# Kernel tuning notes

Hardware: AMD Instinct MI355X
Metric: run time of the kernel (lower is better)

## Reference

```python
import jax, jax.numpy as jnp
import numpy as np

FS = 48000          # sample_rate
C = 343.0           # sound speed
MAX_ORDER = 10
T = 24000           # RIR buffer length
W = 81              # fractional-delay sinc filter length
HALF = W // 2
BETA = 0.9          # wall reflection coefficient
OFFSET = 40.0       # global delay offset (matches shoebox_origin = 40 + fs*d/c)
NEG_SLOPE = 0.01    # torch LeakyReLU default


def _mlp(x, W1, b1, W2, b2, W3, b3):
    h = jax.nn.leaky_relu(x @ W1.T + b1, NEG_SLOPE)
    h = jax.nn.leaky_relu(h @ W2.T + b2, NEG_SLOPE)
    return jax.nn.sigmoid(h @ W3.T + b3)  # [B, 9]


def _image_source_rir(room, mic, src):
    """Batched shoebox image-source RIR synthesis with windowed-sinc scatter.

    room, mic, src: [B, 3]. Returns rir: [B, T].
    """
    B = room.shape[0]
    k = jnp.arange(-MAX_ORDER, MAX_ORDER + 1)          # [K], K = 21
    even = (k % 2 == 0)

    def axis_images(a):
        L = room[:, a:a + 1]                           # [B, 1]
        s = src[:, a:a + 1]                            # [B, 1]
        # even k: k*L + s ; odd k: (k+1)*L - s  (standard 1-D mirror images)
        return jnp.where(even[None, :], k[None, :] * L + s,
                         (k[None, :] + 1) * L - s)     # [B, K]

    ix, iy, iz = axis_images(0), axis_images(1), axis_images(2)
    dx = ix[:, :, None, None] - mic[:, 0, None, None, None]
    dy = iy[:, None, :, None] - mic[:, 1, None, None, None]
    dz = iz[:, None, None, :] - mic[:, 2, None, None, None]
    d = jnp.sqrt(dx * dx + dy * dy + dz * dz)          # [B, K, K, K]

    ka = jnp.abs(k)
    order = (ka[:, None, None] + ka[None, :, None] + ka[None, None, :])  # [K,K,K]

    d = d.reshape(B, -1)                               # [B, K^3]
    order_f = order.reshape(-1).astype(d.dtype)        # [K^3]
    valid_order = order.reshape(-1) <= MAX_ORDER

    amp = jnp.where(valid_order[None, :],
                    (BETA ** order_f)[None, :] / (4.0 * jnp.pi * jnp.maximum(d, 1e-3)),
                    0.0)                               # [B, K^3]

    delay = OFFSET + FS * d / C                        # fractional sample delay
    t0 = jnp.floor(delay)
    frac = delay - t0                                  # grad flows through delay
    t0 = t0.astype(jnp.int32)

    j = jnp.arange(W)
    hann = 0.5 * (1.0 - jnp.cos(2.0 * jnp.pi * j / (W - 1)))
    # windowed fractional-delay sinc taps: [B, K^3, W]
    taps = jnp.sinc((j - HALF)[None, None, :].astype(d.dtype) - frac[..., None]) * hann
    vals = amp[..., None] * taps                       # [B, K^3, W]

    idx = t0[..., None] + (j - HALF)                   # [B, K^3, W]
    in_range = (idx >= 0) & (idx < T)
    vals = jnp.where(in_range, vals, 0.0)
    idx = jnp.clip(idx, 0, T - 1)

    b = jnp.arange(B)[:, None, None]
    return jnp.zeros((B, T), vals.dtype).at[b, idx].add(vals)


def setup_inputs() -> dict:
    key = jax.random.key(0)
    ks = jax.random.split(key, 7)
    B = 128
    inp = {
        "input": jax.random.normal(ks[0], (B, 22), dtype=jnp.float32),
        "W1": jax.random.normal(ks[1], (30, 22), dtype=jnp.float32) * 0.2,
        "b1": jax.random.normal(ks[2], (30,), dtype=jnp.float32) * 0.05,
        "W2": jax.random.normal(ks[3], (20, 30), dtype=jnp.float32) * 0.2,
        "b2": jax.random.normal(ks[4], (20,), dtype=jnp.float32) * 0.05,
        "W3": jax.random.normal(ks[5], (9, 20), dtype=jnp.float32) * 0.2,
        "b3": jax.random.normal(ks[6], (9,), dtype=jnp.float32) * 0.05,
    }
    return inp


def reference(input, W1, b1, W2, b2, W3, b3):
    z = _mlp(input, W1, b1, W2, b2, W3, b3)            # [B, 9] in (0,1)
    room = z[:, 0:3] * 20.0                            # room dims in (0, 20) m
    mic = z[:, 3:6] * room                             # mic inside room
    src = z[:, 6:9] * room                             # source inside room
    rir = _image_source_rir(room, mic, src)            # [B, 24000]
    dist = jnp.linalg.norm(mic - src, axis=1)          # [B]
    origin = 40.0 + FS * dist / C                      # [B]
    return rir, origin
```

## Files before the change

### kernel.cpp

```cpp
#include <hip/hip_runtime.h>
#include <math.h>

#define T_LEN      24000
#define W_LEN      81
#define HALF_W     40
#define NK         21
#define MAXORD     10
#define NIMG_TOTAL 1561
#define NROUNDS    25
#define NB         376
#define GSAMP      128
#define NGRP       188
#define FS_F       48000.0f
#define C_F        343.0f
#define FS_OVER_C  (48000.0f / 343.0f)
#define PI_F       3.14159265358979323846f
#define HSTEP      (2.0f * PI_F / 80.0f)
#define INV_4PI_F  0.07957747154594767f
#define LOG2_BETA  (-0.15200309344504997f)
#define NEG_SLOPE  0.01f

#define HDR_I      384
#define ROW_BYTES  (HDR_I * 4 + 1600 * 16)

struct Table { unsigned int e[NROUNDS * 64]; };
constexpr Table make_table() {
    Table t{};
    int n = 0;
    for (int kx = 0; kx < NK; ++kx)
        for (int ky = 0; ky < NK; ++ky)
            for (int kz = 0; kz < NK; ++kz) {
                int ax = kx >= MAXORD ? kx - MAXORD : MAXORD - kx;
                int ay = ky >= MAXORD ? ky - MAXORD : MAXORD - ky;
                int az = kz >= MAXORD ? kz - MAXORD : MAXORD - kz;
                int order = ax + ay + az;
                if (order <= MAXORD)
                    t.e[n++] = (unsigned)((order << 15) | (kx << 10) | (ky << 5) | kz);
            }
    for (int i = n; i < NROUNDS * 64; ++i) t.e[i] = t.e[n - 1];
    return t;
}
__constant__ Table g_tbl = make_table();

__global__ __launch_bounds__(64)
void rir_prep_kernel(const float* __restrict__ g_in,
                     const float* __restrict__ W1, const float* __restrict__ b1,
                     const float* __restrict__ W2, const float* __restrict__ b2,
                     const float* __restrict__ W3, const float* __restrict__ b3,
                     unsigned char* __restrict__ ws, float* __restrict__ out_origin)
{
    __shared__ float dsq[3 * NK];
    __shared__ float h1[30], h2[20], zb[9], sm_in[22], rms[9];
    __shared__ int counts[NB], offs[NB + 1], cursor[NB];

    const int lane = threadIdx.x;
    const int b    = blockIdx.x;

    for (int i = lane; i < NB; i += 64) { counts[i] = 0; cursor[i] = 0; }

    if (lane < 22) sm_in[lane] = g_in[b * 22 + lane];
    if (lane < 30) {
        float a = b1[lane];
        const float* wp = W1 + lane * 22;
        #pragma unroll
        for (int i = 0; i < 22; ++i) a += sm_in[i] * wp[i];
        h1[lane] = (a >= 0.0f) ? a : NEG_SLOPE * a;
    }
    if (lane < 20) {
        float a = b2[lane];
        const float* wp = W2 + lane * 30;
        #pragma unroll
        for (int i = 0; i < 30; ++i) a += h1[i] * wp[i];
        h2[lane] = (a >= 0.0f) ? a : NEG_SLOPE * a;
    }
    if (lane < 9) {
        float a = b3[lane];
        const float* wp = W3 + lane * 20;
        #pragma unroll
        for (int i = 0; i < 20; ++i) a += h2[i] * wp[i];
        zb[lane] = 1.0f / (1.0f + __expf(-a));
    }
    if (lane < 3) {
        float room = zb[lane] * 20.0f;
        rms[lane]     = room;
        rms[3 + lane] = zb[3 + lane] * room;
        rms[6 + lane] = zb[6 + lane] * room;
    }
    if (lane == 0) {
        float dx = rms[3] - rms[6], dy = rms[4] - rms[7], dz = rms[5] - rms[8];
        out_origin[b] = 40.0f + FS_F * sqrtf(dx * dx + dy * dy + dz * dz) / C_F;
    }
    if (lane < 3 * NK) {
        int a  = lane / NK;
        int kk = (lane - a * NK) - MAXORD;
        float L = rms[a], src = rms[6 + a];
        float img = ((kk & 1) == 0) ? (float)kk * L + src : (float)(kk + 1) * L - src;
        float diff = img - rms[3 + a];
        dsq[lane] = diff * diff;
    }

    for (int r = 0; r < NROUNDS; ++r) {
        int gi = r * 64 + lane;
        unsigned e = g_tbl.e[gi];
        int kzi = e & 31, kyi = (e >> 5) & 31, kxi = (e >> 10) & 31;
        float d   = sqrtf(dsq[kxi] + dsq[NK + kyi] + dsq[2 * NK + kzi]);
        float dly = 40.0f + d * FS_OVER_C;
        int   t0  = (int)floorf(dly);
        bool live = (gi < NIMG_TOTAL) && (t0 - HALF_W < T_LEN);
        if (live) atomicAdd(&counts[t0 >> 6], 1);
    }
    if (lane == 0) {
        int acc = 0;
        for (int s = 0; s < NB; ++s) { offs[s] = acc; acc += counts[s]; }
        offs[NB] = acc;
    }

    unsigned char* rowp = ws + (size_t)b * ROW_BYTES;
    int*    hdr  = (int*)rowp;
    float4* prow = (float4*)(rowp + HDR_I * 4);

    for (int r = 0; r < NROUNDS; ++r) {
        int gi = r * 64 + lane;
        unsigned e = g_tbl.e[gi];
        int kzi = e & 31, kyi = (e >> 5) & 31, kxi = (e >> 10) & 31, order = (int)(e >> 15);
        float d   = sqrtf(dsq[kxi] + dsq[NK + kyi] + dsq[2 * NK + kzi]);
        float dly = 40.0f + d * FS_OVER_C;
        float t0f = floorf(dly);
        int   t0  = (int)t0f;
        bool live = (gi < NIMG_TOTAL) && (t0 - HALF_W < T_LEN);
        if (live) {
            float frac = dly - t0f;
            float amp  = exp2f((float)order * LOG2_BETA) * INV_4PI_F
                         * __builtin_amdgcn_rcpf(fmaxf(d, 0.001f));
            float sp   = __sinf(PI_F * frac);
            int rank = offs[t0 >> 6] + atomicAdd(&cursor[t0 >> 6], 1);
            prow[rank] = make_float4(amp, frac, sp, t0f);
        }
    }

    for (int i = lane; i <= NB; i += 64) hdr[i] = offs[i];
}

__global__ __launch_bounds__(256)
void rir_gather4_kernel(const unsigned char* __restrict__ ws,
                        float* __restrict__ out_rir)
{
    __shared__ float buf[GSAMP];

    const int tid  = threadIdx.x;
    const int lane = tid & 63;
    const int w    = tid >> 6;
    const int grp  = blockIdx.x;
    const int b    = blockIdx.y;
    const int g0   = grp * GSAMP;

    const unsigned char* rowp = ws + (size_t)b * ROW_BYTES;
    const int*    hdr  = (const int*)rowp;
    const float4* prow = (const float4*)(rowp + HDR_I * 4);

    const int blo   = max(g0 - HALF_W, 0) >> 6;
    const int bhi   = min(g0 + GSAMP - 1 + HALF_W, T_LEN + HALF_W - 1) >> 6;
    const int start = hdr[blo];
    const int end   = hdr[bhi + 1];

    if (tid < GSAMP) buf[tid] = 0.0f;
    __syncthreads();

    float acc0 = 0.0f, acc1 = 0.0f;
    const float gf0 = (float)(g0 + lane);

    for (int i = start + w; i < end; i += 4) {
        float4 p = prow[i];
        float n0 = gf0 - p.w;
        float n1 = n0 + 64.0f;

        if (fabsf(n0) <= 40.0f) {
            float x  = n0 - p.y;
            int   ni = (int)n0;
            float sg = (ni & 1) ? p.z : -p.z;
            float sv = (x == 0.0f) ? 1.0f : sg * __builtin_amdgcn_rcpf(PI_F * x);
            float hj = 0.5f - 0.5f * __cosf((n0 + 40.0f) * HSTEP);
            acc0 += p.x * sv * hj;
        }
        if (fabsf(n1) <= 40.0f) {
            float x  = n1 - p.y;
            int   ni = (int)n1;
            float sg = (ni & 1) ? p.z : -p.z;
            float sv = (x == 0.0f) ? 1.0f : sg * __builtin_amdgcn_rcpf(PI_F * x);
            float hj = 0.5f - 0.5f * __cosf((n1 + 40.0f) * HSTEP);
            acc1 += p.x * sv * hj;
        }
    }

    if (acc0 != 0.0f) atomicAdd(&buf[lane], acc0);
    if (acc1 != 0.0f) atomicAdd(&buf[lane + 64], acc1);
    __syncthreads();

    const int g = g0 + tid;
    if (tid < GSAMP && g < T_LEN)
        out_rir[(size_t)b * T_LEN + g] = buf[tid];
}

#define FTS 448
#define FNSLICE 54
__global__ __launch_bounds__(64)
void rir_wave_kernel(const float* __restrict__ g_in,
                     const float* __restrict__ W1, const float* __restrict__ b1,
                     const float* __restrict__ W2, const float* __restrict__ b2,
                     const float* __restrict__ W3, const float* __restrict__ b3,
                     float* __restrict__ out_rir, float* __restrict__ out_origin)
{
    __shared__ __align__(16) float rirw[FTS];
    __shared__ float dsq[3 * NK];
    __shared__ float h1[30], h2[20], zb[9], sm_in[22], rms[9];

    const int lane = threadIdx.x;
    const int s    = blockIdx.x;
    const int b    = blockIdx.y;
    const int lo   = s * FTS;
    const int nout = min(FTS, T_LEN - lo);

    float4* rir4 = (float4*)rirw;
    rir4[lane] = make_float4(0.f, 0.f, 0.f, 0.f);
    if (lane < FTS / 4 - 64) rir4[64 + lane] = make_float4(0.f, 0.f, 0.f, 0.f);

    const float c1p = PI_F * (float)(lane - HALF_W);
    const float hw1 = 0.5f - 0.5f * __cosf((float)lane * HSTEP);
    const float hw2 = 0.5f - 0.5f * __cosf((float)(lane + 64) * HSTEP);
    const float sg  = (lane & 1) ? 1.0f : -1.0f;

    if (lane < 22) sm_in[lane] = g_in[b * 22 + lane];
    if (lane < 30) {
        float a = b1[lane];
        const float* wp = W1 + lane * 22;
        #pragma unroll
        for (int i = 0; i < 22; ++i) a += sm_in[i] * wp[i];
        h1[lane] = (a >= 0.0f) ? a : NEG_SLOPE * a;
    }
    if (lane < 20) {
        float a = b2[lane];
        const float* wp = W2 + lane * 30;
        #pragma unroll
        for (int i = 0; i < 30; ++i) a += h1[i] * wp[i];
        h2[lane] = (a >= 0.0f) ? a : NEG_SLOPE * a;
    }
    if (lane < 9) {
        float a = b3[lane];
        const float* wp = W3 + lane * 20;
        #pragma unroll
        for (int i = 0; i < 20; ++i) a += h2[i] * wp[i];
        zb[lane] = 1.0f / (1.0f + __expf(-a));
    }
    if (lane < 3) {
        float room = zb[lane] * 20.0f;
        rms[lane]     = room;
        rms[3 + lane] = zb[3 + lane] * room;
        rms[6 + lane] = zb[6 + lane] * room;
    }
    if (lane == 0 && s == 0) {
        float dx = rms[3] - rms[6], dy = rms[4] - rms[7], dz = rms[5] - rms[8];
        out_origin[b] = 40.0f + FS_F * sqrtf(dx * dx + dy * dy + dz * dz) / C_F;
    }
    if (lane < 3 * NK) {
        int a  = lane / NK;
        int kk = (lane - a * NK) - MAXORD;
        float L = rms[a], src = rms[6 + a];
        float img = ((kk & 1) == 0) ? (float)kk * L + src : (float)(kk + 1) * L - src;
        float diff = img - rms[3 + a];
        dsq[lane] = diff * diff;
    }

    const float lof = (float)(lo - HALF_W);
    const float hif = (float)(lo + nout - 1 + HALF_W);

    for (int r = 0; r < NROUNDS; ++r) {
        unsigned e = g_tbl.e[r * 64 + lane];
        bool live  = (r * 64 + lane) < NIMG_TOTAL;
        int kzi = e & 31, kyi = (e >> 5) & 31, kxi = (e >> 10) & 31, order = (int)(e >> 15);
        float d    = sqrtf(dsq[kxi] + dsq[NK + kyi] + dsq[2 * NK + kzi]);
        float dlyv = 40.0f + d * FS_OVER_C;
        float t0f  = floorf(dlyv);
        float ampv = exp2f((float)order * LOG2_BETA) * INV_4PI_F
                     * __builtin_amdgcn_rcpf(fmaxf(d, 0.001f));
        bool hit = live && (t0f >= lof) && (t0f <= hif);

        unsigned long long mask = __ballot(hit);
        while (mask) {
            int l0 = __builtin_ctzll(mask); mask &= mask - 1;
            float a0 = __shfl(ampv, l0), d0 = __shfl(dlyv, l0);
            float t0b  = floorf(d0);
            float frac = d0 - t0b;
            float sp   = __sinf(PI_F * frac);
            float pv   = sg * sp;
            int   idx  = (int)t0b - HALF_W + lane - lo;
            float x1p  = c1p - PI_F * frac;
            float sv1  = (x1p == 0.0f) ? 1.0f : pv * __builtin_amdgcn_rcpf(x1p);
            if ((unsigned)idx < (unsigned)nout)
                atomicAdd(&rirw[idx], a0 * sv1 * hw1);
            if (lane < 17) {
                int idx2 = idx + 64;
                float sv2 = pv * __builtin_amdgcn_rcpf(x1p + 64.0f * PI_F);
                if ((unsigned)idx2 < (unsigned)nout)
                    atomicAdd(&rirw[idx2], a0 * sv2 * hw2);
            }
        }
    }

    const int n4 = nout / 4;
    float4* out4 = (float4*)(out_rir + (size_t)b * T_LEN + lo);
    out4[lane] = rir4[lane];
    if (lane + 64 < n4) out4[lane + 64] = rir4[lane + 64];
}

extern "C" void kernel_launch(void* const* d_in, const int* in_sizes, int n_in,
                              void* d_out, int out_size, void* d_ws, size_t ws_size,
                              hipStream_t stream) {
    const float* g_in = (const float*)d_in[0];
    const float* W1   = (const float*)d_in[1];
    const float* b1   = (const float*)d_in[2];
    const float* W2   = (const float*)d_in[3];
    const float* b2   = (const float*)d_in[4];
    const float* W3   = (const float*)d_in[5];
    const float* b3   = (const float*)d_in[6];

    const int B = in_sizes[0] / 22;

    float* out_rir    = (float*)d_out;
    float* out_origin = out_rir + (size_t)B * T_LEN;

    const size_t need_ws = (size_t)B * ROW_BYTES;

    if (ws_size >= need_ws) {
        unsigned char* ws = (unsigned char*)d_ws;
        rir_prep_kernel<<<B, 64, 0, stream>>>(
            g_in, W1, b1, W2, b2, W3, b3, ws, out_origin);
        dim3 grid2(NGRP, B);
        rir_gather4_kernel<<<grid2, 256, 0, stream>>>(ws, out_rir);
    } else {
        dim3 grid(FNSLICE, B);
        rir_wave_kernel<<<grid, 64, 0, stream>>>(
            g_in, W1, b1, W2, b2, W3, b3, out_rir, out_origin);
    }
}
```

Baseline: 73.50 us.

## Widen prep kernel to four waves, parallel scan, and precompute Hann table in gather

The prep kernel now runs with 256 threads, so its rounds are split across four waves, and the serial single-lane prefix sum over the bins is replaced by a wave-level shuffle scan. The record stored per image now holds amp*sin(pi*frac) and amp, which removes a multiply per tap in the gather. The gather kernel builds an 81-entry Hann window in shared memory and looks it up instead of evaluating cosine per tap, and its loop is unrolled by two. Adding __syncthreads barriers fixes ordering that the single-wave version got implicitly, at the cost of barrier overhead and extra shared-memory reads.

```diff
diff --git a/kernel.cpp b/kernel.cpp
--- a/kernel.cpp
+++ b/kernel.cpp
@@ -42,7 +42,7 @@
 }
 __constant__ Table g_tbl = make_table();
 
-__global__ __launch_bounds__(64)
+__global__ __launch_bounds__(256)
 void rir_prep_kernel(const float* __restrict__ g_in,
                      const float* __restrict__ W1, const float* __restrict__ b1,
                      const float* __restrict__ W2, const float* __restrict__ b2,
@@ -53,53 +53,58 @@
     __shared__ float h1[30], h2[20], zb[9], sm_in[22], rms[9];
     __shared__ int counts[NB], offs[NB + 1], cursor[NB];
 
-    const int lane = threadIdx.x;
+    const int tid  = threadIdx.x;
+    const int lane = tid & 63;
+    const int w    = tid >> 6;
     const int b    = blockIdx.x;
 
-    for (int i = lane; i < NB; i += 64) { counts[i] = 0; cursor[i] = 0; }
-
-    if (lane < 22) sm_in[lane] = g_in[b * 22 + lane];
-    if (lane < 30) {
-        float a = b1[lane];
-        const float* wp = W1 + lane * 22;
-        #pragma unroll
-        for (int i = 0; i < 22; ++i) a += sm_in[i] * wp[i];
-        h1[lane] = (a >= 0.0f) ? a : NEG_SLOPE * a;
-    }
-    if (lane < 20) {
-        float a = b2[lane];
-        const float* wp = W2 + lane * 30;
-        #pragma unroll
-        for (int i = 0; i < 30; ++i) a += h1[i] * wp[i];
-        h2[lane] = (a >= 0.0f) ? a : NEG_SLOPE * a;
-    }
-    if (lane < 9) {
-        float a = b3[lane];
-        const float* wp = W3 + lane * 20;
-        #pragma unroll
-        for (int i = 0; i < 20; ++i) a += h2[i] * wp[i];
-        zb[lane] = 1.0f / (1.0f + __expf(-a));
-    }
-    if (lane < 3) {
-        float room = zb[lane] * 20.0f;
-        rms[lane]     = room;
-        rms[3 + lane] = zb[3 + lane] * room;
-        rms[6 + lane] = zb[6 + lane] * room;
-    }
-    if (lane == 0) {
-        float dx = rms[3] - rms[6], dy = rms[4] - rms[7], dz = rms[5] - rms[8];
-        out_origin[b] = 40.0f + FS_F * sqrtf(dx * dx + dy * dy + dz * dz) / C_F;
-    }
-    if (lane < 3 * NK) {
-        int a  = lane / NK;
-        int kk = (lane - a * NK) - MAXORD;
-        float L = rms[a], src = rms[6 + a];
-        float img = ((kk & 1) == 0) ? (float)kk * L + src : (float)(kk + 1) * L - src;
-        float diff = img - rms[3 + a];
-        dsq[lane] = diff * diff;
-    }
-
-    for (int r = 0; r < NROUNDS; ++r) {
+    for (int i = tid; i < NB; i += 256) { counts[i] = 0; cursor[i] = 0; }
+
+    if (w == 0) {
+        if (lane < 22) sm_in[lane] = g_in[b * 22 + lane];
+        if (lane < 30) {
+            float a = b1[lane];
+            const float* wp = W1 + lane * 22;
+            #pragma unroll
+            for (int i = 0; i < 22; ++i) a += sm_in[i] * wp[i];
+            h1[lane] = (a >= 0.0f) ? a : NEG_SLOPE * a;
+        }
+        if (lane < 20) {
+            float a = b2[lane];
+            const float* wp = W2 + lane * 30;
+            #pragma unroll
+            for (int i = 0; i < 30; ++i) a += h1[i] * wp[i];
+            h2[lane] = (a >= 0.0f) ? a : NEG_SLOPE * a;
+        }
+        if (lane < 9) {
+            float a = b3[lane];
+            const float* wp = W3 + lane * 20;
+            #pragma unroll
+            for (int i = 0; i < 20; ++i) a += h2[i] * wp[i];
+            zb[lane] = 1.0f / (1.0f + __expf(-a));
+        }
+        if (lane < 3) {
+            float room = zb[lane] * 20.0f;
+            rms[lane]     = room;
+            rms[3 + lane] = zb[3 + lane] * room;
+            rms[6 + lane] = zb[6 + lane] * room;
+        }
+        if (lane == 0) {
+            float dx = rms[3] - rms[6], dy = rms[4] - rms[7], dz = rms[5] - rms[8];
+            out_origin[b] = 40.0f + FS_F * sqrtf(dx * dx + dy * dy + dz * dz) / C_F;
+        }
+        if (lane < 3 * NK) {
+            int a  = lane / NK;
+            int kk = (lane - a * NK) - MAXORD;
+            float L = rms[a], src = rms[6 + a];
+            float img = ((kk & 1) == 0) ? (float)kk * L + src : (float)(kk + 1) * L - src;
+            float diff = img - rms[3 + a];
+            dsq[lane] = diff * diff;
+        }
+    }
+    __syncthreads();
+
+    for (int r = w; r < NROUNDS; r += 4) {
         int gi = r * 64 + lane;
         unsigned e = g_tbl.e[gi];
         int kzi = e & 31, kyi = (e >> 5) & 31, kxi = (e >> 10) & 31;
@@ -109,17 +114,39 @@
         bool live = (gi < NIMG_TOTAL) && (t0 - HALF_W < T_LEN);
         if (live) atomicAdd(&counts[t0 >> 6], 1);
     }
-    if (lane == 0) {
-        int acc = 0;
-        for (int s = 0; s < NB; ++s) { offs[s] = acc; acc += counts[s]; }
-        offs[NB] = acc;
-    }
+    __syncthreads();
+
+    if (w == 0) {
+        const int base = lane * 6;
+        int c[6], s0 = 0;
+        #pragma unroll
+        for (int j = 0; j < 6; ++j) {
+            int idx = base + j;
+            c[j] = (idx < NB) ? counts[idx] : 0;
+            s0 += c[j];
+        }
+        int incl = s0;
+        #pragma unroll
+        for (int off = 1; off < 64; off <<= 1) {
+            int t = __shfl_up(incl, off);
+            if (lane >= off) incl += t;
+        }
+        int acc = incl - s0;
+        #pragma unroll
+        for (int j = 0; j < 6; ++j) {
+            int idx = base + j;
+            if (idx < NB) offs[idx] = acc;
+            acc += c[j];
+        }
+        if (lane == 63) offs[NB] = acc;
+    }
+    __syncthreads();
 
     unsigned char* rowp = ws + (size_t)b * ROW_BYTES;
     int*    hdr  = (int*)rowp;
     float4* prow = (float4*)(rowp + HDR_I * 4);
 
-    for (int r = 0; r < NROUNDS; ++r) {
+    for (int r = w; r < NROUNDS; r += 4) {
         int gi = r * 64 + lane;
         unsigned e = g_tbl.e[gi];
         int kzi = e & 31, kyi = (e >> 5) & 31, kxi = (e >> 10) & 31, order = (int)(e >> 15);
@@ -134,11 +161,12 @@
                          * __builtin_amdgcn_rcpf(fmaxf(d, 0.001f));
             float sp   = __sinf(PI_F * frac);
             int rank = offs[t0 >> 6] + atomicAdd(&cursor[t0 >> 6], 1);
-            prow[rank] = make_float4(amp, frac, sp, t0f);
-        }
-    }
-
-    for (int i = lane; i <= NB; i += 64) hdr[i] = offs[i];
+            prow[rank] = make_float4(amp * sp, frac, amp, t0f);
+        }
+    }
+    __syncthreads();
+
+    for (int i = tid; i <= NB; i += 256) hdr[i] = offs[i];
 }
 
 __global__ __launch_bounds__(256)
@@ -146,6 +174,7 @@
                         float* __restrict__ out_rir)
 {
     __shared__ float buf[GSAMP];
+    __shared__ float hann[W_LEN + 7];
 
     const int tid  = threadIdx.x;
     const int lane = tid & 63;
@@ -164,11 +193,14 @@
     const int end   = hdr[bhi + 1];
 
     if (tid < GSAMP) buf[tid] = 0.0f;
+    if (tid >= 128 && tid < 128 + W_LEN)
+        hann[tid - 128] = 0.5f - 0.5f * __cosf((float)(tid - 128) * HSTEP);
     __syncthreads();
 
     float acc0 = 0.0f, acc1 = 0.0f;
     const float gf0 = (float)(g0 + lane);
 
+    #pragma unroll 2
     for (int i = start + w; i < end; i += 4) {
         float4 p = prow[i];
         float n0 = gf0 - p.w;
@@ -177,18 +209,16 @@
         if (fabsf(n0) <= 40.0f) {
             float x  = n0 - p.y;
             int   ni = (int)n0;
-            float sg = (ni & 1) ? p.z : -p.z;
-            float sv = (x == 0.0f) ? 1.0f : sg * __builtin_amdgcn_rcpf(PI_F * x);
-            float hj = 0.5f - 0.5f * __cosf((n0 + 40.0f) * HSTEP);
-            acc0 += p.x * sv * hj;
+            float sg = (ni & 1) ? p.x : -p.x;
+            float v  = (x == 0.0f) ? p.z : sg * __builtin_amdgcn_rcpf(PI_F * x);
+            acc0 += v * hann[ni + HALF_W];
         }
         if (fabsf(n1) <= 40.0f) {
             float x  = n1 - p.y;
             int   ni = (int)n1;
-            float sg = (ni & 1) ? p.z : -p.z;
-            float sv = (x == 0.0f) ? 1.0f : sg * __builtin_amdgcn_rcpf(PI_F * x);
-            float hj = 0.5f - 0.5f * __cosf((n1 + 40.0f) * HSTEP);
-            acc1 += p.x * sv * hj;
+            float sg = (ni & 1) ? p.x : -p.x;
+            float v  = (x == 0.0f) ? p.z : sg * __builtin_amdgcn_rcpf(PI_F * x);
+            acc1 += v * hann[ni + HALF_W];
         }
     }
 
@@ -332,7 +362,7 @@
 
     if (ws_size >= need_ws) {
         unsigned char* ws = (unsigned char*)d_ws;
-        rir_prep_kernel<<<B, 64, 0, stream>>>(
+        rir_prep_kernel<<<B, 256, 0, stream>>>(
             g_in, W1, b1, W2, b2, W3, b3, ws, out_origin);
         dim3 grid2(NGRP, B);
         rir_gather4_kernel<<<grid2, 256, 0, stream>>>(ws, out_rir);
```

Measured after the change: 62.89 us. -14.4%, faster.
